# Performance work log

Hardware: AMD Instinct MI355X
Metric: run time of the kernel (lower is better)

The kernel has to match this reference:

```python
import jax, jax.numpy as jnp
import numpy as np

N, E, R, D, DEPTH = 50000, 800000, 1000, 128, 2


def setup_inputs() -> dict:
    key = jax.random.key(0)
    ks = jax.random.split(key, 6)
    features = jax.random.normal(ks[0], (N, D), jnp.float32)
    rel_emb = jax.random.normal(ks[1], (R, D), jnp.float32)
    # adj coalesced by row (torch coalesce sorts indices; values stay aligned)
    src = jnp.sort(jax.random.randint(ks[2], (E,), 0, N))
    dst = jax.random.randint(ks[3], (E,), 0, N)
    adj = jnp.stack([src, dst]).astype(jnp.int64)
    # one relation per triple: row index = triple id, col = relation id
    r_index = jnp.stack([jnp.arange(E), jax.random.randint(ks[4], (E,), 0, R)]).astype(jnp.int64)
    r_val = jax.random.uniform(ks[5], (E,), jnp.float32)
    attn_kernels = jax.random.normal(jax.random.fold_in(key, 7), (DEPTH, D), jnp.float32) * 0.1
    return {"features": features, "rel_emb": rel_emb, "adj": adj, "r_index": r_index,
            "r_val": r_val, "triple_size": E, "rel_size": R, "node_size": N,
            "attn_kernels": attn_kernels}


def _layer(features, rel_emb, adj, r_index, r_val, triple_size, node_size, attn_k):
    row = adj[0]
    neighs = features[adj[1]]                                   # [E, D] gather
    # sparse.mm(tri_rel, rel_emb): sum_j r_val * rel_emb[col] per triple row
    tri_rel = jax.ops.segment_sum(r_val[:, None] * rel_emb[r_index[1]],
                                  r_index[0], num_segments=triple_size)  # [E, D]
    nrm = jnp.linalg.norm(tri_rel, axis=1, keepdims=True)
    tri_rel = tri_rel / jnp.maximum(nrm, 1e-12)                 # F.normalize(p=2)
    # Householder-style reflection
    neighs = neighs - 2.0 * jnp.sum(neighs * tri_rel, axis=1, keepdims=True) * tri_rel
    att = tri_rel @ attn_k                                      # [E]
    # sparse row-wise softmax over edges grouped by destination row
    m = jax.ops.segment_max(att, row, num_segments=node_size)
    e = jnp.exp(att - m[row])
    s = jax.ops.segment_sum(e, row, num_segments=node_size)
    att = e / s[row]
    new_features = jax.ops.segment_sum(neighs * att[:, None], row,
                                       num_segments=node_size)  # [N, D] scatter
    return jnp.tanh(new_features)


def reference(features, rel_emb, adj, r_index, r_val, triple_size, rel_size, node_size, attn_kernels):
    features = jnp.tanh(features)
    outputs = [features]
    for l in range(attn_kernels.shape[0]):
        features = _layer(features, rel_emb, adj, r_index, r_val,
                          triple_size, node_size, attn_kernels[l])
        outputs.append(features)
    return jnp.concatenate(outputs, axis=-1)                    # [N, D*(depth+1)]
```

## Files before the change

kernel.cpp:

```cpp
#include <hip/hip_runtime.h>
#include <hip/hip_bf16.h>
#include <math.h>

#define N_NODES   50000
#define N_EDGES   800000
#define N_REL     1000
#define DIM       128
#define DEPTH_L   2
#define OUT_STRIDE (DIM * (DEPTH_L + 1))

typedef _Float16 h2 __attribute__((ext_vector_type(2)));

#if defined(__has_builtin)
#if __has_builtin(__builtin_amdgcn_fdot2)
#define FDOT2(a, b, c) __builtin_amdgcn_fdot2((a), (b), (c), false)
#endif
#endif
#ifndef FDOT2
#define FDOT2(a, b, c) ((c) + (float)(a).x * (float)(b).x + (float)(a).y * (float)(b).y)
#endif

__device__ __forceinline__ float fast_tanh(float x) {
    float cx = fminf(fmaxf(x, -15.f), 15.f);
    float e = __expf(2.f * cx);
    return (e - 1.f) * __frcp_rn(e + 1.f);
}

__global__ __launch_bounds__(64) void prep_rel_kernel(
    const float* __restrict__ rel_emb,
    const float* __restrict__ attn_k,
    _Float16* __restrict__ rhat,
    float* __restrict__ er0, float* __restrict__ er1)
{
    int r = blockIdx.x;
    int lane = threadIdx.x;
    if (r == N_REL) {
        rhat[(size_t)r * DIM + lane]      = (_Float16)0.f;
        rhat[(size_t)r * DIM + lane + 64] = (_Float16)0.f;
        if (lane == 0) { er0[N_REL] = 1.f; er1[N_REL] = 1.f; }
        return;
    }
    float v0 = rel_emb[r * DIM + lane];
    float v1 = rel_emb[r * DIM + lane + 64];
    float ss = v0 * v0 + v1 * v1;
    #pragma unroll
    for (int o = 32; o >= 1; o >>= 1) ss += __shfl_xor(ss, o);
    float inv = 1.0f / fmaxf(sqrtf(ss), 1e-12f);
    float t0 = v0 * inv, t1 = v1 * inv;
    rhat[(size_t)r * DIM + lane]      = (_Float16)t0;
    rhat[(size_t)r * DIM + lane + 64] = (_Float16)t1;
    #pragma unroll
    for (int l = 0; l < DEPTH_L; ++l) {
        float d = t0 * attn_k[l * DIM + lane] + t1 * attn_k[l * DIM + lane + 64];
        #pragma unroll
        for (int o = 32; o >= 1; o >>= 1) d += __shfl_xor(d, o);
        if (lane == 0) {
            if (l == 0) er0[r] = __expf(d); else er1[r] = __expf(d);
        }
    }
}

__global__ __launch_bounds__(256) void rowptr_kernel(
    const int* __restrict__ src, int* __restrict__ rp,
    float* __restrict__ s0, float* __restrict__ s1)
{
    int n = blockIdx.x * blockDim.x + threadIdx.x;
    if (n > N_NODES) return;
    int lo = 0, hi = N_EDGES;
    while (lo < hi) {
        int mid = (lo + hi) >> 1;
        if (src[mid] < n) lo = mid + 1; else hi = mid;
    }
    rp[n] = lo;
    if (n < N_NODES) { s0[n] = 0.f; s1[n] = 0.f; }
}

__global__ __launch_bounds__(256) void tanh0_kernel(
    const float* __restrict__ feat, float* __restrict__ out,
    _Float16* __restrict__ fs0)
{
    int i = blockIdx.x * blockDim.x + threadIdx.x;
    if (i >= N_NODES * 32) return;
    int n = i >> 5;
    int j = i & 31;
    float4 v = reinterpret_cast<const float4*>(feat + (size_t)n * DIM)[j];
    float4 o;
    o.x = fast_tanh(v.x); o.y = fast_tanh(v.y);
    o.z = fast_tanh(v.z); o.w = fast_tanh(v.w);
    reinterpret_cast<float4*>(out + (size_t)n * OUT_STRIDE)[j] = o;
    h2 p0; p0.x = (_Float16)o.x; p0.y = (_Float16)o.y;
    h2 p1; p1.x = (_Float16)o.z; p1.y = (_Float16)o.w;
    uint2 u;
    u.x = __builtin_bit_cast(unsigned, p0);
    u.y = __builtin_bit_cast(unsigned, p1);
    reinterpret_cast<uint2*>(fs0 + (size_t)n * DIM)[j] = u;
}

__global__ __launch_bounds__(256) void sum_einfo_kernel(
    const int* __restrict__ src, const int* __restrict__ dst,
    const int* __restrict__ relid, const float* __restrict__ rval,
    const float* __restrict__ er0, const float* __restrict__ er1,
    float* __restrict__ s0, float* __restrict__ s1,
    uint2* __restrict__ einfo2)
{
    int e = blockIdx.x * 256 + threadIdx.x;
    if (e >= N_EDGES) return;
    int lane = threadIdx.x & 63;
    int sn = src[e];
    int r = (rval[e] == 0.f) ? N_REL : relid[e];
    float x0 = er0[r], x1 = er1[r];

    h2 ep; ep.x = (_Float16)x0; ep.y = (_Float16)x1;
    einfo2[e] = make_uint2((unsigned)dst[e] | ((unsigned)r << 16),
                           __builtin_bit_cast(unsigned, ep));

    #pragma unroll
    for (int off = 1; off < 64; off <<= 1) {
        float y0 = __shfl_up(x0, off);
        float y1 = __shfl_up(x1, off);
        int   sp = __shfl_up(sn, off);
        if (lane >= off && sp == sn) { x0 += y0; x1 += y1; }
    }
    int snext = __shfl_down(sn, 1);
    bool lastlane = (lane == 63) || (e == N_EDGES - 1) || (snext != sn);
    if (lastlane) {
        atomicAdd(&s0[sn], x0);
        atomicAdd(&s1[sn], x1);
    }
}

template<int L>
__global__ __launch_bounds__(128) void layer_fused_kernel(
    const _Float16* __restrict__ fs_in,
    float* __restrict__ fout,
    _Float16* __restrict__ fs_out,
    const uint2* __restrict__ einfo2,
    const int* __restrict__ rp,
    const float* __restrict__ s_l,
    const _Float16* __restrict__ rhat)
{
    int wid  = threadIdx.x >> 6;
    int lane = threadIdx.x & 63;
    int node = blockIdx.x * 2 + wid;
    if (node >= N_NODES) return;
    int start = rp[node], end = rp[node + 1];
    int g = lane >> 3;
    int q = lane & 7;

    float inv_s = 1.0f / s_l[node];

    const char* fbase = (const char*)fs_in + 32 * q;
    const char* tbase = (const char*)rhat  + 32 * q;
    int g0 = (lane >> 3) & 1, g1 = (lane >> 4) & 1, g2 = (lane >> 5) & 1;

    h2 a2[8];
    #pragma unroll
    for (int i = 0; i < 8; ++i) { a2[i].x = (_Float16)0.f; a2[i].y = (_Float16)0.f; }

    for (int e0 = start; e0 < end; e0 += 16) {
        int eL = end - 1;
        int ea = e0 + g;
        int ca = (ea < eL) ? ea : eL;
        uint2 ia = einfo2[ca];
        int eb = e0 + 8 + g;
        int cb = (eb < eL) ? eb : eL;
        uint2 ib = einfo2[cb];

        unsigned dnA = ia.x & 0xffffu, rlA = ia.x >> 16;
        unsigned dnB = ib.x & 0xffffu, rlB = ib.x >> 16;
        const uint4* hpA = reinterpret_cast<const uint4*>(fbase + (size_t)dnA * 256);
        const uint4* tpA = reinterpret_cast<const uint4*>(tbase + (size_t)rlA * 256);
        const uint4* hpB = reinterpret_cast<const uint4*>(fbase + (size_t)dnB * 256);
        const uint4* tpB = reinterpret_cast<const uint4*>(tbase + (size_t)rlB * 256);
        uint4 hA0 = hpA[0], hA1 = hpA[1];
        uint4 tA0 = tpA[0], tA1 = tpA[1];
        uint4 hB0 = hpB[0], hB1 = hpB[1];
        uint4 tB0 = tpB[0], tB1 = tpB[1];

        h2 epA = __builtin_bit_cast(h2, ia.y);
        h2 epB = __builtin_bit_cast(h2, ib.y);
        float erA = (float)((L == 0) ? epA.x : epA.y);
        float erB = (float)((L == 0) ? epB.x : epB.y);
        float wAf = (ea < end) ? erA * inv_s : 0.f;
        float wBf = (eb < end) ? erB * inv_s : 0.f;

        __builtin_amdgcn_sched_barrier(0);

        {
            h2 hh[8], tt[8];
            hh[0] = __builtin_bit_cast(h2, hA0.x); hh[1] = __builtin_bit_cast(h2, hA0.y);
            hh[2] = __builtin_bit_cast(h2, hA0.z); hh[3] = __builtin_bit_cast(h2, hA0.w);
            hh[4] = __builtin_bit_cast(h2, hA1.x); hh[5] = __builtin_bit_cast(h2, hA1.y);
            hh[6] = __builtin_bit_cast(h2, hA1.z); hh[7] = __builtin_bit_cast(h2, hA1.w);
            tt[0] = __builtin_bit_cast(h2, tA0.x); tt[1] = __builtin_bit_cast(h2, tA0.y);
            tt[2] = __builtin_bit_cast(h2, tA0.z); tt[3] = __builtin_bit_cast(h2, tA0.w);
            tt[4] = __builtin_bit_cast(h2, tA1.x); tt[5] = __builtin_bit_cast(h2, tA1.y);
            tt[6] = __builtin_bit_cast(h2, tA1.z); tt[7] = __builtin_bit_cast(h2, tA1.w);
            float d0 = 0.f, d1 = 0.f;
            #pragma unroll
            for (int p = 0; p < 8; p += 2) {
                d0 = FDOT2(hh[p],     tt[p],     d0);
                d1 = FDOT2(hh[p + 1], tt[p + 1], d1);
            }
            float d = d0 + d1;
            d += __shfl_xor(d, 1);
            d += __shfl_xor(d, 2);
            d += __shfl_xor(d, 4);
            float cf = -2.f * wAf * d;
            _Float16 wh  = (_Float16)wAf;
            _Float16 cfh = (_Float16)cf;
            h2 wv; wv.x = wh;  wv.y = wh;
            h2 cv; cv.x = cfh; cv.y = cfh;
            #pragma unroll
            for (int p = 0; p < 8; ++p) {
                a2[p] = hh[p] * wv + a2[p];
                a2[p] = tt[p] * cv + a2[p];
            }
        }

        {
            h2 hh[8], tt[8];
            hh[0] = __builtin_bit_cast(h2, hB0.x); hh[1] = __builtin_bit_cast(h2, hB0.y);
            hh[2] = __builtin_bit_cast(h2, hB0.z); hh[3] = __builtin_bit_cast(h2, hB0.w);
            hh[4] = __builtin_bit_cast(h2, hB1.x); hh[5] = __builtin_bit_cast(h2, hB1.y);
            hh[6] = __builtin_bit_cast(h2, hB1.z); hh[7] = __builtin_bit_cast(h2, hB1.w);
            tt[0] = __builtin_bit_cast(h2, tB0.x); tt[1] = __builtin_bit_cast(h2, tB0.y);
            tt[2] = __builtin_bit_cast(h2, tB0.z); tt[3] = __builtin_bit_cast(h2, tB0.w);
            tt[4] = __builtin_bit_cast(h2, tB1.x); tt[5] = __builtin_bit_cast(h2, tB1.y);
            tt[6] = __builtin_bit_cast(h2, tB1.z); tt[7] = __builtin_bit_cast(h2, tB1.w);
            float d0 = 0.f, d1 = 0.f;
            #pragma unroll
            for (int p = 0; p < 8; p += 2) {
                d0 = FDOT2(hh[p],     tt[p],     d0);
                d1 = FDOT2(hh[p + 1], tt[p + 1], d1);
            }
            float d = d0 + d1;
            d += __shfl_xor(d, 1);
            d += __shfl_xor(d, 2);
            d += __shfl_xor(d, 4);
            float cf = -2.f * wBf * d;
            _Float16 wh  = (_Float16)wBf;
            _Float16 cfh = (_Float16)cf;
            h2 wv; wv.x = wh;  wv.y = wh;
            h2 cv; cv.x = cfh; cv.y = cfh;
            #pragma unroll
            for (int p = 0; p < 8; ++p) {
                a2[p] = hh[p] * wv + a2[p];
                a2[p] = tt[p] * cv + a2[p];
            }
        }
    }

    h2 b1[4];
    #pragma unroll
    for (int k = 0; k < 4; ++k) {
        h2 keep = g0 ? a2[2*k + 1] : a2[2*k];
        h2 send = g0 ? a2[2*k] : a2[2*k + 1];
        unsigned su = __shfl_xor(__builtin_bit_cast(unsigned, send), 8);
        b1[k] = keep + __builtin_bit_cast(h2, su);
    }
    h2 b2[2];
    #pragma unroll
    for (int m = 0; m < 2; ++m) {
        h2 keep = g1 ? b1[2*m + 1] : b1[2*m];
        h2 send = g1 ? b1[2*m] : b1[2*m + 1];
        unsigned su = __shfl_xor(__builtin_bit_cast(unsigned, send), 16);
        b2[m] = keep + __builtin_bit_cast(h2, su);
    }
    h2 c;
    {
        h2 keep = g2 ? b2[1] : b2[0];
        h2 send = g2 ? b2[0] : b2[1];
        unsigned su = __shfl_xor(__builtin_bit_cast(unsigned, send), 32);
        c = keep + __builtin_bit_cast(h2, su);
    }

    float y0 = fast_tanh((float)c.x), y1 = fast_tanh((float)c.y);
    int dimo = 16 * q + 2 * g;
    *reinterpret_cast<float2*>(fout + (size_t)node * OUT_STRIDE + dimo)
        = make_float2(y0, y1);
    if (L == 0) {
        h2 pr; pr.x = (_Float16)y0; pr.y = (_Float16)y1;
        *reinterpret_cast<h2*>(fs_out + (size_t)node * DIM + dimo) = pr;
    }
}

extern "C" void kernel_launch(void* const* d_in, const int* in_sizes, int n_in,
                              void* d_out, int out_size, void* d_ws, size_t ws_size,
                              hipStream_t stream)
{
    const float* features = (const float*)d_in[0];
    const float* rel_emb  = (const float*)d_in[1];
    const int*   adj      = (const int*)d_in[2];
    const int*   r_index  = (const int*)d_in[3];
    const float* r_val    = (const float*)d_in[4];
    const float* attn_k   = (const float*)d_in[8];
    float* out = (float*)d_out;

    const int* src   = adj;
    const int* dst   = adj + N_EDGES;
    const int* relid = r_index + N_EDGES;

    char* base = (char*)d_ws;
    _Float16* rhat = (_Float16*)base;
    float*    er0  = (float*)(base + 256256);
    float*    er1  = (float*)(base + 260264);
    int*      rp   = (int*)(base + 264272);
    float*    s0   = (float*)(base + 464288);
    float*    s1   = (float*)(base + 664288);
    uint2*    einfo2 = (uint2*)(base + 864288);
    _Float16* fs0  = (_Float16*)(base + 864288 + (size_t)N_EDGES * 8);
    _Float16* fs1  = fs0 + (size_t)N_NODES * DIM;

    prep_rel_kernel<<<N_REL + 1, 64, 0, stream>>>(rel_emb, attn_k, rhat, er0, er1);
    rowptr_kernel<<<(N_NODES + 1 + 255) / 256, 256, 0, stream>>>(src, rp, s0, s1);
    tanh0_kernel<<<(N_NODES * 32 + 255) / 256, 256, 0, stream>>>(features, out, fs0);
    sum_einfo_kernel<<<(N_EDGES + 255) / 256, 256, 0, stream>>>(
        src, dst, relid, r_val, er0, er1, s0, s1, einfo2);

    layer_fused_kernel<0><<<(N_NODES + 1) / 2, 128, 0, stream>>>(
        fs0, out + 1 * DIM, fs1, einfo2, rp, s0, rhat);
    layer_fused_kernel<1><<<(N_NODES + 1) / 2, 128, 0, stream>>>(
        fs1, out + 2 * DIM, fs0, einfo2, rp, s1, rhat);
}
```

Measured before the change: 114.1 us.

## Software-pipeline edge gather loop and broadcast edge info via wave shuffles

```diff
diff --git a/kernel.cpp b/kernel.cpp
--- a/kernel.cpp
+++ b/kernel.cpp
@@ -157,45 +157,48 @@
     #pragma unroll
     for (int i = 0; i < 8; ++i) { a2[i].x = (_Float16)0.f; a2[i].y = (_Float16)0.f; }
 
-    for (int e0 = start; e0 < end; e0 += 16) {
-        int eL = end - 1;
-        int ea = e0 + g;
-        int ca = (ea < eL) ? ea : eL;
-        uint2 ia = einfo2[ca];
-        int eb = e0 + 8 + g;
-        int cb = (eb < eL) ? eb : eL;
-        uint2 ib = einfo2[cb];
-
-        unsigned dnA = ia.x & 0xffffu, rlA = ia.x >> 16;
-        unsigned dnB = ib.x & 0xffffu, rlB = ib.x >> 16;
-        const uint4* hpA = reinterpret_cast<const uint4*>(fbase + (size_t)dnA * 256);
-        const uint4* tpA = reinterpret_cast<const uint4*>(tbase + (size_t)rlA * 256);
-        const uint4* hpB = reinterpret_cast<const uint4*>(fbase + (size_t)dnB * 256);
-        const uint4* tpB = reinterpret_cast<const uint4*>(tbase + (size_t)rlB * 256);
-        uint4 hA0 = hpA[0], hA1 = hpA[1];
-        uint4 tA0 = tpA[0], tA1 = tpA[1];
-        uint4 hB0 = hpB[0], hB1 = hpB[1];
-        uint4 tB0 = tpB[0], tB1 = tpB[1];
-
-        h2 epA = __builtin_bit_cast(h2, ia.y);
-        h2 epB = __builtin_bit_cast(h2, ib.y);
-        float erA = (float)((L == 0) ? epA.x : epA.y);
-        float erB = (float)((L == 0) ? epB.x : epB.y);
-        float wAf = (ea < end) ? erA * inv_s : 0.f;
-        float wBf = (eb < end) ? erB * inv_s : 0.f;
-
-        __builtin_amdgcn_sched_barrier(0);
-
-        {
+    if (start < end) {
+        int deg = end - start;
+        bool small = (deg <= 64);
+        unsigned eix = 0, eiy = 0;
+        if (small) {
+            int lc = start + lane; if (lc > end - 1) lc = end - 1;
+            uint2 et = einfo2[lc];
+            eix = et.x; eiy = et.y;
+        }
+
+        auto LOADC = [&](int e0, uint4& h0, uint4& h1, uint4& t0, uint4& t1,
+                         float& w) {
+            unsigned ax, ay;
+            if (small) {
+                int slot = e0 - start + g;
+                ax = __shfl(eix, slot);
+                ay = __shfl(eiy, slot);
+            } else {
+                int ec = e0 + g; if (ec > end - 1) ec = end - 1;
+                uint2 et = einfo2[ec];
+                ax = et.x; ay = et.y;
+            }
+            unsigned dn = ax & 0xffffu, rl = ax >> 16;
+            const uint4* hp = reinterpret_cast<const uint4*>(fbase + (size_t)dn * 256);
+            const uint4* tp = reinterpret_cast<const uint4*>(tbase + (size_t)rl * 256);
+            h0 = hp[0]; h1 = hp[1];
+            t0 = tp[0]; t1 = tp[1];
+            h2 ep = __builtin_bit_cast(h2, ay);
+            float er = (float)((L == 0) ? ep.x : ep.y);
+            w = (e0 + g < end) ? er * inv_s : 0.f;
+        };
+
+        auto COMPUTEC = [&](uint4 h0, uint4 h1, uint4 t0, uint4 t1, float wf) {
             h2 hh[8], tt[8];
-            hh[0] = __builtin_bit_cast(h2, hA0.x); hh[1] = __builtin_bit_cast(h2, hA0.y);
-            hh[2] = __builtin_bit_cast(h2, hA0.z); hh[3] = __builtin_bit_cast(h2, hA0.w);
-            hh[4] = __builtin_bit_cast(h2, hA1.x); hh[5] = __builtin_bit_cast(h2, hA1.y);
-            hh[6] = __builtin_bit_cast(h2, hA1.z); hh[7] = __builtin_bit_cast(h2, hA1.w);
-            tt[0] = __builtin_bit_cast(h2, tA0.x); tt[1] = __builtin_bit_cast(h2, tA0.y);
-            tt[2] = __builtin_bit_cast(h2, tA0.z); tt[3] = __builtin_bit_cast(h2, tA0.w);
-            tt[4] = __builtin_bit_cast(h2, tA1.x); tt[5] = __builtin_bit_cast(h2, tA1.y);
-            tt[6] = __builtin_bit_cast(h2, tA1.z); tt[7] = __builtin_bit_cast(h2, tA1.w);
+            hh[0] = __builtin_bit_cast(h2, h0.x); hh[1] = __builtin_bit_cast(h2, h0.y);
+            hh[2] = __builtin_bit_cast(h2, h0.z); hh[3] = __builtin_bit_cast(h2, h0.w);
+            hh[4] = __builtin_bit_cast(h2, h1.x); hh[5] = __builtin_bit_cast(h2, h1.y);
+            hh[6] = __builtin_bit_cast(h2, h1.z); hh[7] = __builtin_bit_cast(h2, h1.w);
+            tt[0] = __builtin_bit_cast(h2, t0.x); tt[1] = __builtin_bit_cast(h2, t0.y);
+            tt[2] = __builtin_bit_cast(h2, t0.z); tt[3] = __builtin_bit_cast(h2, t0.w);
+            tt[4] = __builtin_bit_cast(h2, t1.x); tt[5] = __builtin_bit_cast(h2, t1.y);
+            tt[6] = __builtin_bit_cast(h2, t1.z); tt[7] = __builtin_bit_cast(h2, t1.w);
             float d0 = 0.f, d1 = 0.f;
             #pragma unroll
             for (int p = 0; p < 8; p += 2) {
@@ -206,8 +209,8 @@
             d += __shfl_xor(d, 1);
             d += __shfl_xor(d, 2);
             d += __shfl_xor(d, 4);
-            float cf = -2.f * wAf * d;
-            _Float16 wh  = (_Float16)wAf;
+            float cf = -2.f * wf * d;
+            _Float16 wh  = (_Float16)wf;
             _Float16 cfh = (_Float16)cf;
             h2 wv; wv.x = wh;  wv.y = wh;
             h2 cv; cv.x = cfh; cv.y = cfh;
@@ -216,38 +219,27 @@
                 a2[p] = hh[p] * wv + a2[p];
                 a2[p] = tt[p] * cv + a2[p];
             }
-        }
-
-        {
-            h2 hh[8], tt[8];
-            hh[0] = __builtin_bit_cast(h2, hB0.x); hh[1] = __builtin_bit_cast(h2, hB0.y);
-            hh[2] = __builtin_bit_cast(h2, hB0.z); hh[3] = __builtin_bit_cast(h2, hB0.w);
-            hh[4] = __builtin_bit_cast(h2, hB1.x); hh[5] = __builtin_bit_cast(h2, hB1.y);
-            hh[6] = __builtin_bit_cast(h2, hB1.z); hh[7] = __builtin_bit_cast(h2, hB1.w);
-            tt[0] = __builtin_bit_cast(h2, tB0.x); tt[1] = __builtin_bit_cast(h2, tB0.y);
-            tt[2] = __builtin_bit_cast(h2, tB0.z); tt[3] = __builtin_bit_cast(h2, tB0.w);
-            tt[4] = __builtin_bit_cast(h2, tB1.x); tt[5] = __builtin_bit_cast(h2, tB1.y);
-            tt[6] = __builtin_bit_cast(h2, tB1.z); tt[7] = __builtin_bit_cast(h2, tB1.w);
-            float d0 = 0.f, d1 = 0.f;
-            #pragma unroll
-            for (int p = 0; p < 8; p += 2) {
-                d0 = FDOT2(hh[p],     tt[p],     d0);
-                d1 = FDOT2(hh[p + 1], tt[p + 1], d1);
-            }
-            float d = d0 + d1;
-            d += __shfl_xor(d, 1);
-            d += __shfl_xor(d, 2);
-            d += __shfl_xor(d, 4);
-            float cf = -2.f * wBf * d;
-            _Float16 wh  = (_Float16)wBf;
-            _Float16 cfh = (_Float16)cf;
-            h2 wv; wv.x = wh;  wv.y = wh;
-            h2 cv; cv.x = cfh; cv.y = cfh;
-            #pragma unroll
-            for (int p = 0; p < 8; ++p) {
-                a2[p] = hh[p] * wv + a2[p];
-                a2[p] = tt[p] * cv + a2[p];
-            }
+        };
+
+        uint4 hA0, hA1, tA0, tA1; float wA;
+        uint4 hB0, hB1, tB0, tB1; float wB;
+        LOADC(start, hA0, hA1, tA0, tA1, wA);
+        int e = start;
+        while (true) {
+            int e2 = e + 8;
+            bool moreB = (e2 < end);
+            if (moreB) LOADC(e2, hB0, hB1, tB0, tB1, wB);
+            __builtin_amdgcn_sched_barrier(0);
+            COMPUTEC(hA0, hA1, tA0, tA1, wA);
+            e = e2;
+            if (!moreB) break;
+            int e3 = e + 8;
+            bool moreA = (e3 < end);
+            if (moreA) LOADC(e3, hA0, hA1, tA0, tA1, wA);
+            __builtin_amdgcn_sched_barrier(0);
+            COMPUTEC(hB0, hB1, tB0, tB1, wB);
+            e = e3;
+            if (!moreA) break;
         }
     }
 
```

Measured after the change: 113.2 us. No clear change (-0.8%).
